# Performance work log

Hardware: AMD Instinct MI355X
Metric: run time of the kernel (lower is better)

The kernel has to match this reference:

```python
import jax, jax.numpy as jnp
import numpy as np


def conv1x1(x, w, b):
    # x: (B,C,H,W), w: (Cout,Cin), b: (Cout,) -- 1x1 conv == channel matmul
    return jnp.einsum('bchw,oc->bohw', x, w) + b[None, :, None, None]


def spatial_gate(q_feat, k_feat, scale):
    # Faithful to: matmul over flattened (B*HW, C) x (C, B*HW), then
    # max over keys, mean over the batch axis, softmax over spatial dims.
    B, C, H, W = q_feat.shape
    q = q_feat.reshape(B, C, H * W).transpose(0, 2, 1).reshape(B * H * W, C)
    k = k_feat.reshape(B, C, H * W).transpose(1, 0, 2).reshape(C, B * H * W)
    s = (q @ k).reshape(B * H * W, B, H * W)          # (BHW, B, HW)
    m = jnp.mean(jnp.max(s, axis=-1), axis=-1)        # (BHW,)
    w = jax.nn.softmax(m.reshape(B, H * W) * scale, axis=-1)
    return w.reshape(B, 1, H, W)


def setup_inputs() -> dict:
    key = jax.random.key(0)
    ks = jax.random.split(key, 10)
    C = 256
    shp = (8, C, 32, 32)
    inp = {
        'x4': jax.random.normal(ks[0], shp, jnp.float32),
        'x3': jax.random.normal(ks[1], shp, jnp.float32),
        'wq': jax.random.normal(ks[2], (C, C), jnp.float32) * 0.02,
        'bq': jnp.zeros((C,), jnp.float32),
        'wk': jax.random.normal(ks[3], (C, C), jnp.float32) * 0.02,
        'bk': jnp.zeros((C,), jnp.float32),
        'wv': jax.random.normal(ks[4], (C, C), jnp.float32) * 0.02,
        'bv': jnp.zeros((C,), jnp.float32),
        'w128': jax.random.normal(ks[5], (128, C), jnp.float32) * 0.02,
        'b128': jnp.zeros((128,), jnp.float32),
    }
    return inp


def reference(x4, x3, wq, bq, wk, bk, wv, bv, w128, b128):
    C = x4.shape[1]
    scale = 1.0 / (C ** 0.5)
    # shared QKV 1x1 convs applied to both inputs
    aq = conv1x1(x4, wq, bq)
    ak = conv1x1(x4, wk, bk)
    av = conv1x1(x4, wv, bv)
    bq_f = conv1x1(x3, wq, bq)
    bk_f = conv1x1(x3, wk, bk)
    bv_f = conv1x1(x3, wv, bv)
    # four gating branches: self-self (a), self-self (b), cross a->b, cross b->a
    a_x4 = conv1x1(spatial_gate(aq, ak, scale) * av, w128, b128)
    b_x3 = conv1x1(spatial_gate(bq_f, bk_f, scale) * bv_f, w128, b128)
    x43 = conv1x1(spatial_gate(aq, bk_f, scale) * bv_f, w128, b128)
    x34 = conv1x1(spatial_gate(bq_f, ak, scale) * av, w128, b128)
    # cat order: [x34, a_x4] then [x43, b_x3]
    ab_cat = jnp.concatenate([x34, a_x4, x43, b_x3], axis=1)  # (B,512,H,W)
    # Block2D loop: block class undefined in source; surrogate = identity
    # (ab12 = concat of the two chunks == ab_cat), applied depth=4 times.
    ab12 = ab_cat
    ab12 = ab_cat * ab12
    ab_avg = jnp.mean(ab12, axis=(2, 3), keepdims=True)        # (B,512,1,1)
    ab = jax.nn.softmax(ab_avg, axis=-1)   # softmax over size-1 axis -> ones
    final = ab * ab_cat
    return final
```

## Files before the change

kernel.cpp:

```cpp
#include <hip/hip_runtime.h>

typedef unsigned short ushort_t;
typedef unsigned char uchar_t;
typedef __attribute__((ext_vector_type(8))) short bf16x8;
typedef __attribute__((ext_vector_type(4))) float f32x4;
typedef __attribute__((ext_vector_type(16))) float f32x16;
typedef __attribute__((ext_vector_type(8))) int v8i;

__device__ __forceinline__ unsigned short f2bf(float f) {
  union { float f; unsigned int u; } v; v.f = f;
  unsigned int r = v.u + 0x7FFFu + ((v.u >> 16) & 1u);
  return (unsigned short)(r >> 16);
}

__device__ __forceinline__ float bf2f(unsigned short u) {
  union { unsigned int i; float f; } v; v.i = ((unsigned int)u) << 16;
  return v.f;
}

__device__ __forceinline__ void gl_lds16(const void* gsrc, void* ldst) {
  __builtin_amdgcn_global_load_lds(
      (const __attribute__((address_space(1))) void*)gsrc,
      (__attribute__((address_space(3))) void*)ldst, 16, 0, 0);
}

__device__ __forceinline__ int frag_idx(int oc, int ci) {
  return (((oc>>4)*8 + (ci>>5))<<9) + ((((ci>>3)&3)*16 + (oc&15))<<3) + (ci&7);
}

__global__ __launch_bounds__(256) void k1_weights(
    const float* __restrict__ wq, const float* __restrict__ bq,
    const float* __restrict__ wk, const float* __restrict__ bk,
    const float* __restrict__ wv, const float* __restrict__ bv,
    const float* __restrict__ w128,
    ushort_t* __restrict__ Wf, float* __restrict__ bias_all)
{
  const int ci = threadIdx.x;
  const int oc = blockIdx.x;
  if (oc < 512) {
    const float v = (oc < 256) ? wq[oc*256 + ci] : wk[(oc-256)*256 + ci];
    Wf[frag_idx(oc, ci)] = f2bf(v);
    if (ci == 0) bias_all[oc] = (oc < 256) ? bq[oc] : bk[oc-256];
  } else {
    const int o = oc - 512;
    const float* wr = w128 + (size_t)o*256;
    float a = 0.f;
    for (int co = 0; co < 256; co++) a += wr[co] * wv[co*256 + ci];
    Wf[frag_idx(oc, ci)] = f2bf(a);
    if (ci == 0) {
      float s = 0.f;
      for (int co = 0; co < 256; co++) s += wr[co] * bv[co];
      bias_all[oc] = s;
    }
  }
}

__global__ __launch_bounds__(256) void k2_features(
    const float* __restrict__ x4, const float* __restrict__ x3,
    const ushort_t* __restrict__ Wf, const float* __restrict__ bias_all,
    uchar_t* __restrict__ Qf8, uchar_t* __restrict__ Kf8, float* __restrict__ V)
{
  __shared__ ushort_t Af[32*512];
  __shared__ ushort_t Wl[2][32*512];
  __shared__ ushort_t Lt[64*72];

  const int tid = threadIdx.x;
  const int w = tid >> 6, lane = tid & 63;
  const int mrow = lane & 15, quad = lane >> 4;
  const int ln31 = lane & 31, half = lane >> 5;

  const int px0 = blockIdx.x * 64;
  const int src = px0 >> 13, b = (px0 >> 10) & 7, hw0 = px0 & 1023;
  const float* xp = (src ? x3 : x4) + (size_t)b*262144;

  const int ot0 = blockIdx.y * 5;

  for (int kb = 0; kb < 8; kb++)
    gl_lds16(Wf + ((size_t)((ot0*4 + w)*8 + kb)<<9) + lane*8,
             &Wl[ot0&1][(w*8+kb)*512]);

  {
    const int hw = hw0 + w*16 + mrow;
    for (int kb = 0; kb < 8; kb++) {
      const int ch0 = kb*32 + quad*8;
      bf16x8 pk;
      #pragma unroll
      for (int j = 0; j < 8; j++)
        ((ushort_t*)&pk)[j] = f2bf(xp[(size_t)(ch0 + j)*1024 + hw]);
      *(bf16x8*)&Af[(w*8 + kb)*512 + lane*8] = pk;
    }
  }
  __syncthreads();

  for (int ot = ot0; ot < ot0 + 5; ot++) {
    const int nbuf = (ot+1) & 1, cbuf = ot & 1;
    if (ot + 1 < ot0 + 5) {
      for (int kb = 0; kb < 8; kb++)
        gl_lds16(Wf + ((size_t)(((ot+1)*4 + w)*8 + kb)<<9) + lane*8,
                 &Wl[nbuf][(w*8+kb)*512]);
      asm volatile("s_waitcnt vmcnt(8)" ::: "memory");
    } else {
      asm volatile("s_waitcnt vmcnt(0)" ::: "memory");
    }

    f32x4 acc[4];
    #pragma unroll
    for (int lg = 0; lg < 4; lg++) acc[lg] = (f32x4){0.f,0.f,0.f,0.f};
    #pragma unroll
    for (int kb = 0; kb < 8; kb++) {
      const bf16x8 a = *(const bf16x8*)&Wl[cbuf][(w*8 + kb)*512 + lane*8];
      #pragma unroll
      for (int lg = 0; lg < 4; lg++) {
        const bf16x8 bx = *(const bf16x8*)&Af[(lg*8 + kb)*512 + lane*8];
        acc[lg] = __builtin_amdgcn_mfma_f32_16x16x32_bf16(a, bx, acc[lg], 0, 0, 0);
      }
    }
    const int ocl = w*16 + quad*4;
    const float4 bias4 = *(const float4*)&bias_all[ot*64 + ocl];

    if (ot < 8) {
      __syncthreads();
      #pragma unroll
      for (int lg = 0; lg < 4; lg++) {
        const int px = lg*16 + mrow;
        ushort4 pk;
        pk.x = f2bf(acc[lg][0] + bias4.x);
        pk.y = f2bf(acc[lg][1] + bias4.y);
        pk.z = f2bf(acc[lg][2] + bias4.z);
        pk.w = f2bf(acc[lg][3] + bias4.w);
        *(ushort4*)&Lt[px*72 + ocl] = pk;
      }
      __syncthreads();
      const int g = w >> 1, e = w & 1;
      const int row = g*32 + ln31;
      const ushort_t* lp = &Lt[row*72 + e*32 + half*8];
      float fl[8], fh[8];
      #pragma unroll
      for (int j = 0; j < 8; j++) { fl[j] = bf2f(lp[j]); fh[j] = bf2f(lp[16+j]); }
      int w0 = __builtin_amdgcn_cvt_pk_fp8_f32(fl[0], fl[1], 0, 0);
      w0     = __builtin_amdgcn_cvt_pk_fp8_f32(fl[2], fl[3], w0, 1);
      int w1 = __builtin_amdgcn_cvt_pk_fp8_f32(fl[4], fl[5], 0, 0);
      w1     = __builtin_amdgcn_cvt_pk_fp8_f32(fl[6], fl[7], w1, 1);
      int w2 = __builtin_amdgcn_cvt_pk_fp8_f32(fh[0], fh[1], 0, 0);
      w2     = __builtin_amdgcn_cvt_pk_fp8_f32(fh[2], fh[3], w2, 1);
      int w3 = __builtin_amdgcn_cvt_pk_fp8_f32(fh[4], fh[5], 0, 0);
      w3     = __builtin_amdgcn_cvt_pk_fp8_f32(fh[6], fh[7], w3, 1);
      uchar_t* dst = (ot < 4) ? Qf8 : Kf8;
      const size_t chunk = (size_t)((px0>>5) + g)*8 + (ot&3)*2 + e;
      int4 pk4; pk4.x = w0; pk4.y = w1; pk4.z = w2; pk4.w = w3;
      *(int4*)(dst + (chunk<<10) + lane*16) = pk4;
    } else {
      const int ocv0 = (ot-8)*64 + ocl;
      float* vb = V + (((size_t)(src*8 + b)*128) << 10) + hw0;
      #pragma unroll
      for (int lg = 0; lg < 4; lg++) {
        vb[(size_t)(ocv0+0)*1024 + lg*16 + mrow] = acc[lg][0] + bias4.x;
        vb[(size_t)(ocv0+1)*1024 + lg*16 + mrow] = acc[lg][1] + bias4.y;
        vb[(size_t)(ocv0+2)*1024 + lg*16 + mrow] = acc[lg][2] + bias4.z;
        vb[(size_t)(ocv0+3)*1024 + lg*16 + mrow] = acc[lg][3] + bias4.w;
      }
    }
  }
}

__global__ __launch_bounds__(512, 2) void k3_smax(
    const uchar_t* __restrict__ Qf8, const uchar_t* __restrict__ Kf8,
    float* __restrict__ Pm)
{
  __shared__ __align__(16) uchar_t Kl[2][32768];

  const int tid = threadIdx.x;
  const int bt = blockIdx.x >> 5;
  const int rt = blockIdx.x & 31;
  const int w = tid >> 6, lane = tid & 63;
  const int ln31 = lane & 31, half = lane >> 5;

  const int rgb = rt*16 + w*2;
  const int ph = (blockIdx.x & 1)*4;

  #pragma unroll
  for (int q = 0; q < 4; q++) {
    const int c = w*4 + q;
    const int cg = bt*32 + ph*4 + (c>>3);
    gl_lds16(Kf8 + (((size_t)cg*8 + (c&7))<<10) + lane*16, &Kl[0][c*1024]);
  }

  v8i qa[2][4];
  #pragma unroll
  for (int rg = 0; rg < 2; rg++)
    #pragma unroll
    for (int u = 0; u < 4; u++) {
      const int4 p0 = *(const int4*)(Qf8 + (((size_t)(rgb + rg)*8 + 2*u+0)<<10) + lane*16);
      const int4 p1 = *(const int4*)(Qf8 + (((size_t)(rgb + rg)*8 + 2*u+1)<<10) + lane*16);
      qa[rg][u] = (v8i){p0.x, p0.y, p0.z, p0.w, p1.x, p1.y, p1.z, p1.w};
    }

  f32x16 zv;
  #pragma unroll
  for (int i = 0; i < 16; i++) zv[i] = 0.f;
  f32x16 rmax[2];
  #pragma unroll
  for (int rg = 0; rg < 2; rg++)
    #pragma unroll
    for (int i = 0; i < 16; i++) rmax[rg][i] = -3.4e38f;

  #pragma unroll 1
  for (int s = 0; s < 8; s++) {
    __syncthreads();
    if (s < 7) {
      const int sn = (s + 1 + ph) & 7;
      #pragma unroll
      for (int q = 0; q < 4; q++) {
        const int c = w*4 + q;
        const int cg = bt*32 + sn*4 + (c>>3);
        gl_lds16(Kf8 + (((size_t)cg*8 + (c&7))<<10) + lane*16,
                 &Kl[(s+1)&1][c*1024]);
      }
    }
    const uchar_t* kl = Kl[s & 1];
    #pragma unroll
    for (int cgl = 0; cgl < 4; cgl++) {
      f32x16 a0 = zv, a1 = zv;
      #pragma unroll
      for (int u = 0; u < 4; u++) {
        const int4 b0 = *(const int4*)&kl[(cgl*8 + 2*u+0)*1024 + lane*16];
        const int4 b1 = *(const int4*)&kl[(cgl*8 + 2*u+1)*1024 + lane*16];
        const v8i bu = (v8i){b0.x, b0.y, b0.z, b0.w, b1.x, b1.y, b1.z, b1.w};
        a0 = __builtin_amdgcn_mfma_scale_f32_32x32x64_f8f6f4(
            qa[0][u], bu, a0, 0, 0, 0, 0x7F7F7F7F, 0, 0x7F7F7F7F);
        a1 = __builtin_amdgcn_mfma_scale_f32_32x32x64_f8f6f4(
            qa[1][u], bu, a1, 0, 0, 0, 0x7F7F7F7F, 0, 0x7F7F7F7F);
      }
      #pragma unroll
      for (int i = 0; i < 16; i++) {
        rmax[0][i] = fmaxf(rmax[0][i], a0[i]);
        rmax[1][i] = fmaxf(rmax[1][i], a1[i]);
      }
    }
  }

  #pragma unroll
  for (int rg = 0; rg < 2; rg++) {
    #pragma unroll
    for (int e = 0; e < 16; e++) {
      float v = rmax[rg][e];
      v = fmaxf(v, __shfl_xor(v, 1));
      v = fmaxf(v, __shfl_xor(v, 2));
      v = fmaxf(v, __shfl_xor(v, 4));
      v = fmaxf(v, __shfl_xor(v, 8));
      v = fmaxf(v, __shfl_xor(v, 16));
      if (ln31 == 0) {
        const int row = rt*512 + w*64 + rg*32 + (e&3) + 8*(e>>2) + 4*half;
        Pm[(size_t)bt*16384 + row] = v;
      }
    }
  }
}

__global__ __launch_bounds__(256) void k5_out(
    const float* __restrict__ V, const float* __restrict__ Pm,
    const float* __restrict__ b128, float* __restrict__ out)
{
  __shared__ float xw[2][4];
  const int tid = threadIdx.x;
  const int ch = blockIdx.x & 511, b = blockIdx.x >> 9;
  const int blk = ch >> 7, o = ch & 127;
  const int gidx = (blk == 0) ? 2 : (blk == 1) ? 0 : (blk == 2) ? 1 : 3;
  const int src = (blk >= 2) ? 1 : 0;
  const int qset = gidx >> 1, side = gidx & 1;

  const float4* Pm4 = (const float4*)(Pm + (size_t)side*8*16384 + qset*8192 + b*1024);
  float4 l = {0.f, 0.f, 0.f, 0.f};
  #pragma unroll
  for (int t = 0; t < 8; t++) {
    const float4 p = Pm4[t*4096 + tid];
    l.x += p.x; l.y += p.y; l.z += p.z; l.w += p.w;
  }
  const float sc = 0.125f * 0.0625f;
  l.x *= sc; l.y *= sc; l.z *= sc; l.w *= sc;

  const int w = tid >> 6, lane = tid & 63;
  float m = fmaxf(fmaxf(l.x, l.y), fmaxf(l.z, l.w));
  #pragma unroll
  for (int d = 1; d < 64; d <<= 1) m = fmaxf(m, __shfl_xor(m, d));
  if (lane == 0) xw[0][w] = m;
  __syncthreads();
  m = fmaxf(fmaxf(xw[0][0], xw[0][1]), fmaxf(xw[0][2], xw[0][3]));

  float4 e;
  e.x = expf(l.x - m); e.y = expf(l.y - m);
  e.z = expf(l.z - m); e.w = expf(l.w - m);
  float s = e.x + e.y + e.z + e.w;
  #pragma unroll
  for (int d = 1; d < 64; d <<= 1) s += __shfl_xor(s, d);
  if (lane == 0) xw[1][w] = s;
  __syncthreads();
  s = xw[1][0] + xw[1][1] + xw[1][2] + xw[1][3];
  const float inv = 1.f / s;

  const int hw0 = tid << 2;
  const float4 v = *(const float4*)&V[((size_t)((src*8 + b)*128 + o) << 10) + hw0];
  const float bias = b128[o];
  float4 r;
  r.x = e.x*inv*v.x + bias; r.y = e.y*inv*v.y + bias;
  r.z = e.z*inv*v.z + bias; r.w = e.w*inv*v.w + bias;
  *(float4*)&out[((size_t)(b*512 + ch) << 10) + hw0] = r;
}

extern "C" void kernel_launch(void* const* d_in, const int* in_sizes, int n_in,
                              void* d_out, int out_size, void* d_ws, size_t ws_size,
                              hipStream_t stream)
{
  const float* x4   = (const float*)d_in[0];
  const float* x3   = (const float*)d_in[1];
  const float* wq   = (const float*)d_in[2];
  const float* bq   = (const float*)d_in[3];
  const float* wk   = (const float*)d_in[4];
  const float* bk   = (const float*)d_in[5];
  const float* wv   = (const float*)d_in[6];
  const float* bv   = (const float*)d_in[7];
  const float* w128 = (const float*)d_in[8];
  const float* b128 = (const float*)d_in[9];
  float* out = (float*)d_out;

  char* ws = (char*)d_ws;
  uchar_t*  Qf8 = (uchar_t*)ws;  ws += (size_t)512*8*1024;
  uchar_t*  Kf8 = (uchar_t*)ws;  ws += (size_t)512*8*1024;
  float*    V   = (float*)ws;    ws += (size_t)2*8*128*1024*4;
  float*    Pm  = (float*)ws;    ws += (size_t)16*16384*4;
  ushort_t* Wf  = (ushort_t*)ws; ws += (size_t)640*256*2;
  float* bias_all = (float*)ws;

  k1_weights <<<640,          256, 0, stream>>>(wq, bq, wk, bk, wv, bv, w128, Wf, bias_all);
  k2_features<<<dim3(256, 2), 256, 0, stream>>>(x4, x3, Wf, bias_all, Qf8, Kf8, V);
  k3_smax    <<<512,          512, 0, stream>>>(Qf8, Kf8, Pm);
  k5_out     <<<4096,         256, 0, stream>>>(V, Pm, b128, out);
}
```

Baseline: 182.1 us.

## Read K fragments directly from global memory in max-score kernel, drop LDS staging

The k3_smax kernel no longer stages K tiles through a double-buffered 64KB LDS buffer with barriers. Each wave now loads its K fragments straight from global memory (relying on L2/cache reuse across the 8 waves) and iterates over all 32 column groups. This removes __syncthreads and the LDS footprint, which may raise occupancy, but each wave now issues redundant global loads and the per-block rotation phase is dropped. Separately, the projection kernel's wait count on the weight prefetch is relaxed from vmcnt(8) to vmcnt(32).

```diff
diff --git a/kernel.cpp b/kernel.cpp
--- a/kernel.cpp
+++ b/kernel.cpp
@@ -98,7 +98,7 @@
       for (int kb = 0; kb < 8; kb++)
         gl_lds16(Wf + ((size_t)(((ot+1)*4 + w)*8 + kb)<<9) + lane*8,
                  &Wl[nbuf][(w*8+kb)*512]);
-      asm volatile("s_waitcnt vmcnt(8)" ::: "memory");
+      asm volatile("s_waitcnt vmcnt(32)" ::: "memory");
     } else {
       asm volatile("s_waitcnt vmcnt(0)" ::: "memory");
     }
@@ -167,8 +167,6 @@
     const uchar_t* __restrict__ Qf8, const uchar_t* __restrict__ Kf8,
     float* __restrict__ Pm)
 {
-  __shared__ __align__(16) uchar_t Kl[2][32768];
-
   const int tid = threadIdx.x;
   const int bt = blockIdx.x >> 5;
   const int rt = blockIdx.x & 31;
@@ -176,14 +174,6 @@
   const int ln31 = lane & 31, half = lane >> 5;
 
   const int rgb = rt*16 + w*2;
-  const int ph = (blockIdx.x & 1)*4;
-
-  #pragma unroll
-  for (int q = 0; q < 4; q++) {
-    const int c = w*4 + q;
-    const int cg = bt*32 + ph*4 + (c>>3);
-    gl_lds16(Kf8 + (((size_t)cg*8 + (c&7))<<10) + lane*16, &Kl[0][c*1024]);
-  }
 
   v8i qa[2][4];
   #pragma unroll
@@ -204,38 +194,26 @@
     #pragma unroll
     for (int i = 0; i < 16; i++) rmax[rg][i] = -3.4e38f;
 
+  const uchar_t* kbase = Kf8 + ((size_t)(bt*32*8) << 10) + lane*16;
+
   #pragma unroll 1
-  for (int s = 0; s < 8; s++) {
-    __syncthreads();
-    if (s < 7) {
-      const int sn = (s + 1 + ph) & 7;
-      #pragma unroll
-      for (int q = 0; q < 4; q++) {
-        const int c = w*4 + q;
-        const int cg = bt*32 + sn*4 + (c>>3);
-        gl_lds16(Kf8 + (((size_t)cg*8 + (c&7))<<10) + lane*16,
-                 &Kl[(s+1)&1][c*1024]);
-      }
-    }
-    const uchar_t* kl = Kl[s & 1];
-    #pragma unroll
-    for (int cgl = 0; cgl < 4; cgl++) {
-      f32x16 a0 = zv, a1 = zv;
-      #pragma unroll
-      for (int u = 0; u < 4; u++) {
-        const int4 b0 = *(const int4*)&kl[(cgl*8 + 2*u+0)*1024 + lane*16];
-        const int4 b1 = *(const int4*)&kl[(cgl*8 + 2*u+1)*1024 + lane*16];
-        const v8i bu = (v8i){b0.x, b0.y, b0.z, b0.w, b1.x, b1.y, b1.z, b1.w};
-        a0 = __builtin_amdgcn_mfma_scale_f32_32x32x64_f8f6f4(
-            qa[0][u], bu, a0, 0, 0, 0, 0x7F7F7F7F, 0, 0x7F7F7F7F);
-        a1 = __builtin_amdgcn_mfma_scale_f32_32x32x64_f8f6f4(
-            qa[1][u], bu, a1, 0, 0, 0, 0x7F7F7F7F, 0, 0x7F7F7F7F);
-      }
-      #pragma unroll
-      for (int i = 0; i < 16; i++) {
-        rmax[0][i] = fmaxf(rmax[0][i], a0[i]);
-        rmax[1][i] = fmaxf(rmax[1][i], a1[i]);
-      }
+  for (int cg = 0; cg < 32; cg++) {
+    const uchar_t* kc = kbase + ((size_t)(cg*8) << 10);
+    f32x16 a0 = zv, a1 = zv;
+    #pragma unroll
+    for (int u = 0; u < 4; u++) {
+      const int4 b0 = *(const int4*)(kc + (2*u+0)*1024);
+      const int4 b1 = *(const int4*)(kc + (2*u+1)*1024);
+      const v8i bu = (v8i){b0.x, b0.y, b0.z, b0.w, b1.x, b1.y, b1.z, b1.w};
+      a0 = __builtin_amdgcn_mfma_scale_f32_32x32x64_f8f6f4(
+          qa[0][u], bu, a0, 0, 0, 0, 0x7F7F7F7F, 0, 0x7F7F7F7F);
+      a1 = __builtin_amdgcn_mfma_scale_f32_32x32x64_f8f6f4(
+          qa[1][u], bu, a1, 0, 0, 0, 0x7F7F7F7F, 0, 0x7F7F7F7F);
+    }
+    #pragma unroll
+    for (int i = 0; i < 16; i++) {
+      rmax[0][i] = fmaxf(rmax[0][i], a0[i]);
+      rmax[1][i] = fmaxf(rmax[1][i], a1[i]);
     }
   }
 
```

Result: slower. 192.4 us (+5.7%).
